# Kernel tuning notes

Measured on AMD Instinct MI355X. Metric: run time of the kernel, lower is better.

Reference implementation:

```python
import jax, jax.numpy as jnp
import numpy as np


def setup_inputs() -> dict:
    key = jax.random.key(0)
    k1, k2 = jax.random.split(key)
    B, C, M, N = 4, 3, 4096, 8192
    query = jax.random.normal(k1, (B, C, M), dtype=jnp.float32)
    points = jax.random.normal(k2, (B, C, N), dtype=jnp.float32)
    return {"k": 16, "query": query, "points": points}


def reference(k, query, points):
    # query: BxCxM, points: BxCxN  (trans=True path of original module)
    q = jnp.swapaxes(query, 1, 2)   # BxMxC
    p = jnp.swapaxes(points, 1, 2)  # BxNxC
    # squared L2 distances (FAISS GpuIndexFlatL2): BxMxN
    q2 = jnp.sum(q * q, axis=-1, keepdims=True)           # BxMx1
    p2 = jnp.sum(p * p, axis=-1)[:, None, :]              # Bx1xN
    dist = q2 + p2 - 2.0 * jnp.einsum('bmc,bnc->bmn', q, p)
    # k smallest distances, sorted ascending (FAISS sorts results)
    _, index_batch = jax.lax.top_k(-dist, k)              # BxMxK int32
    index_batch = index_batch.astype(jnp.int64) if index_batch.dtype != jnp.int64 else index_batch
    # gather neighbor coordinates: points BxCxN, idx BxMxK -> BxCxMxK
    neighbor_points = jax.vmap(lambda pts, idx: pts[:, idx])(points, index_batch)
    return neighbor_points, index_batch
```

## Files before the change

### kernel.cpp

```cpp
#include <hip/hip_runtime.h>
#include <stdint.h>

#define BQ 4
#define CC 3
#define MM 4096
#define NN 8192
#define KK 16
#define NP_OFF (BQ*CC*MM*KK)
#define BLOCK 512
#define ROWS 32
#define CHUNK 1024
#define NCH (NN/CHUNK)
#define EPSA 4e-3f

typedef __attribute__((ext_vector_type(8)))  short   short8;
typedef __attribute__((ext_vector_type(8)))  __bf16  bf16x8;
typedef __attribute__((ext_vector_type(16))) float   f32x16;
typedef unsigned int u32;
typedef unsigned short u16;

#define BT_PER_BATCH 256
#define AT_PER_BATCH 128
#define A_OFF (BQ*BT_PER_BATCH*64)

__device__ __forceinline__ float rfl(float x) {
    return __uint_as_float((unsigned)__builtin_amdgcn_readfirstlane((int)__float_as_uint(x)));
}
__device__ __forceinline__ unsigned mapf(float f) {
    unsigned u = __float_as_uint(f);
    return (u & 0x80000000u) ? ~u : (u | 0x80000000u);
}
__device__ __forceinline__ float unmapf(unsigned u) {
    unsigned b = (u & 0x80000000u) ? (u & 0x7fffffffu) : ~u;
    return __uint_as_float(b);
}
__device__ __forceinline__ u16 bfh(float f) {
    unsigned u = __float_as_uint(f);
    return (u16)((u + 0x7fffu + ((u >> 16) & 1u)) >> 16);
}
__device__ __forceinline__ float bff(u16 h) {
    return __uint_as_float(((unsigned)h) << 16);
}

__device__ __forceinline__ f32x16 mfma3216(short8 a, short8 b, f32x16 c) {
    return __builtin_amdgcn_mfma_f32_32x32x16_bf16(
        __builtin_bit_cast(bf16x8, a), __builtin_bit_cast(bf16x8, b), c, 0, 0, 0);
}

__device__ __forceinline__ void gl_lds16(const void* g, void* l) {
    __builtin_amdgcn_global_load_lds(
        (const __attribute__((address_space(1))) u32*)g,
        (__attribute__((address_space(3))) u32*)l, 16, 0, 0);
}

__global__ void pack_kernel(const float* __restrict__ query,
                            const float* __restrict__ points,
                            short8* __restrict__ ws)
{
    const int lane = threadIdx.x;
    const int bid  = blockIdx.x;
    const int hi   = lane >> 5;
    const int j    = lane & 31;
    short8 v = {0,0,0,0,0,0,0,0};
    if (bid < BQ*BT_PER_BATCH) {
        const int b = bid >> 8, tile = bid & 255;
        const int n = tile*32 + j;
        const float* pb = points + b*(CC*NN);
        float px = pb[n], py = pb[NN+n], pz = pb[2*NN+n];
        float pw = -0.5f*(px*px + py*py + pz*pz);
        u16 xh=bfh(px), yh=bfh(py), zh=bfh(pz), wh=bfh(pw);
        u16 xl=bfh(px-bff(xh)), yl=bfh(py-bff(yh)), zl=bfh(pz-bff(zh)), wl=bfh(pw-bff(wh));
        if (hi == 0) { v[0]=(short)xh; v[1]=(short)xh; v[2]=(short)xl; v[3]=(short)yh;
                       v[4]=(short)zl; v[5]=(short)wh; v[6]=(short)wl; v[7]=0; }
        else         { v[0]=(short)yh; v[1]=(short)yl; v[2]=(short)zh; v[3]=(short)zh; }
        ws[bid*64 + lane] = v;
    } else {
        const int t2 = bid - BQ*BT_PER_BATCH;
        const int b = t2 >> 7, rt = t2 & 127;
        const int m = rt*32 + j;
        const float* qb = query + b*(CC*MM);
        float qx = qb[m], qy = qb[MM+m], qz = qb[2*MM+m];
        u16 xh=bfh(qx), yh=bfh(qy), zh=bfh(qz);
        u16 xl=bfh(qx-bff(xh)), yl=bfh(qy-bff(yh)), zl=bfh(qz-bff(zh));
        const u16 ONE = 0x3F80u;
        if (hi == 0) { v[0]=(short)xh; v[1]=(short)xl; v[2]=(short)xh; v[3]=(short)yh;
                       v[4]=(short)zh; v[5]=(short)ONE; v[6]=(short)ONE; v[7]=0; }
        else         { v[0]=(short)yl; v[1]=(short)yh; v[2]=(short)zh; v[3]=(short)zl; }
        ws[A_OFF + t2*64 + lane] = v;
    }
}

__global__ __launch_bounds__(BLOCK, 4) void knn_kernel(
    const float* __restrict__ query,
    const float* __restrict__ points,
    const short8* __restrict__ ws,
    float* __restrict__ out)
{
    __shared__ short8 bpk[2][2048];
    __shared__ unsigned aux[ROWS][64];
    __shared__ unsigned scnt[ROWS];
    __shared__ unsigned rcbits[ROWS];

    const int tid  = threadIdx.x;
    const int lane = tid & 63;
    const int wv   = tid >> 6;
    const int col  = lane & 31;
    const int hi4  = (lane >> 5) << 2;
    const int bid  = blockIdx.x;
    const int b    = bid >> 7;
    const int rt   = bid & 127;
    const int rb   = rt * 32;

    const float* pb = points + b*(CC*NN);
    const float* qb = query  + b*(CC*MM);

    #pragma unroll
    for (int i = 0; i < 4; ++i) ((unsigned*)aux)[i*BLOCK + tid] = 0u;
    if (tid < ROWS) scnt[tid] = 0u;

    const short8 af = ws[A_OFF + (b*AT_PER_BATCH + rt)*64 + lane];
    const f32x16 zf = {0.f,0.f,0.f,0.f,0.f,0.f,0.f,0.f,
                       0.f,0.f,0.f,0.f,0.f,0.f,0.f,0.f};

    float rm0[16], rm1[16];
    #pragma unroll
    for (int j = 0; j < 16; ++j) { rm0[j] = -__builtin_inff(); rm1[j] = -__builtin_inff(); }

    const short8* Bb = ws + (size_t)b * (BT_PER_BATCH*64);

    auto stage = [&](int ch, int bi) {
        #pragma unroll
        for (int i = 0; i < 4; ++i) {
            int idx = i*BLOCK + tid;
            gl_lds16(&Bb[ch*2048 + idx], &bpk[bi][idx]);
        }
    };

    auto comp1 = [&](int bi) {
        #pragma unroll
        for (int p = 0; p < 2; ++p) {
            short8 b0 = bpk[bi][(wv*4 + p)*64 + lane];
            short8 b1 = bpk[bi][(wv*4 + p + 2)*64 + lane];
            f32x16 d0 = mfma3216(af, b0, zf);
            f32x16 d1 = mfma3216(af, b1, zf);
            #pragma unroll
            for (int j = 0; j < 16; ++j) {
                float t = fmaxf(d0[j], d1[j]);
                if (p == 0) rm0[j] = fmaxf(rm0[j], t);
                else        rm1[j] = fmaxf(rm1[j], t);
            }
        }
    };

    stage(0, 0);
    #pragma unroll 1
    for (int ch = 0; ch < NCH; ch += 2) {
        __syncthreads();
        if (ch + 1 < NCH) stage(ch + 1, 1);
        comp1(0);
        __syncthreads();
        if (ch + 2 < NCH) stage(ch + 2, 0);
        if (ch + 1 < NCH) comp1(1);
    }

    #pragma unroll
    for (int j = 0; j < 16; ++j) {
        int row = ((j & 3) + 8*(j >> 2)) + hi4;
        atomicMax(&aux[row][col],      mapf(rm0[j]));
        atomicMax(&aux[row][col + 32], mapf(rm1[j]));
    }
    __syncthreads();
    stage(0, 0);

    #pragma unroll
    for (int rr = 0; rr < 4; ++rr) {
        int row = wv*4 + rr;
        unsigned v = aux[row][lane];
        #pragma unroll
        for (int k = 2; k <= 64; k <<= 1) {
            #pragma unroll
            for (int jj = k >> 1; jj > 0; jj >>= 1) {
                unsigned o = __shfl_xor(v, jj, 64);
                bool keepmin = (((lane & jj) == 0) == ((lane & k) == 0));
                v = keepmin ? (v < o ? v : o) : (v > o ? v : o);
            }
        }
        unsigned tb = __shfl(v, 48, 64);
        if (lane == 0) rcbits[row] = __float_as_uint(unmapf(tb) - EPSA);
    }
    __syncthreads();

    float rcv[16];
    #pragma unroll
    for (int j = 0; j < 16; ++j)
        rcv[j] = __uint_as_float(rcbits[((j & 3) + 8*(j >> 2)) + hi4]);

    auto comp2 = [&](int ch, int bi) {
        #pragma unroll
        for (int p = 0; p < 2; ++p) {
            short8 b0 = bpk[bi][(wv*4 + p)*64 + lane];
            short8 b1 = bpk[bi][(wv*4 + p + 2)*64 + lane];
            f32x16 d0 = mfma3216(af, b0, zf);
            f32x16 d1 = mfma3216(af, b1, zf);
            unsigned n0 = (unsigned)(ch*CHUNK + (wv*4 + p)*32 + col);
            #pragma unroll
            for (int j = 0; j < 16; ++j) {
                float t = fmaxf(d0[j], d1[j]);
                if (t >= rcv[j]) {
                    int row = ((j & 3) + 8*(j >> 2)) + hi4;
                    if (d0[j] >= rcv[j]) {
                        unsigned pos = atomicAdd(&scnt[row], 1u);
                        if (pos < 64u) aux[row][pos] = n0;
                    }
                    if (d1[j] >= rcv[j]) {
                        unsigned pos = atomicAdd(&scnt[row], 1u);
                        if (pos < 64u) aux[row][pos] = n0 + 64u;
                    }
                }
            }
        }
    };

    #pragma unroll 1
    for (int ch = 0; ch < NCH; ch += 2) {
        __syncthreads();
        if (ch + 1 < NCH) stage(ch + 1, 1);
        comp2(ch, 0);
        __syncthreads();
        if (ch + 2 < NCH) stage(ch + 2, 0);
        if (ch + 1 < NCH) comp2(ch + 1, 1);
    }
    __syncthreads();

    #pragma unroll 1
    for (int rr = 0; rr < 4; ++rr) {
        int row = wv*4 + rr;
        int m   = rb + row;
        float ex = rfl(qb[m]);
        float ey = rfl(qb[MM + m]);
        float ez = rfl(qb[2*MM + m]);
        float eq2 = rfl(__fadd_rn(__fadd_rn(__fmul_rn(ex,ex), __fmul_rn(ey,ey)),
                                  __fmul_rn(ez,ez)));
        unsigned c = scnt[row]; if (c > 64u) c = 64u;
        unsigned kb = 0xffffffffu, id = 0xffffffffu;
        if (lane < (int)c) {
            id = aux[row][lane];
            float px = pb[id], py = pb[NN + id], pz = pb[2*NN + id];
            float p2 = __fadd_rn(__fadd_rn(__fmul_rn(px,px), __fmul_rn(py,py)),
                                 __fmul_rn(pz,pz));
            float dot = __builtin_fmaf(ez, pz,
                         __builtin_fmaf(ey, py, __fmul_rn(ex, px)));
            float d = __fsub_rn(__fadd_rn(eq2, p2), __fmul_rn(2.0f, dot));
            unsigned fb = __float_as_uint(d);
            kb = (fb & 0x80000000u) ? ~fb : (fb | 0x80000000u);
        }
        #pragma unroll
        for (int k = 2; k <= 64; k <<= 1) {
            #pragma unroll
            for (int j = k >> 1; j > 0; j >>= 1) {
                unsigned ok = __shfl_xor(kb, j, 64);
                unsigned oi = __shfl_xor(id, j, 64);
                bool takeMin  = (((lane & j) == 0) == ((lane & k) == 0));
                bool selfLess = (kb < ok) || (kb == ok && id < oi);
                if (selfLess != takeMin) { kb = ok; id = oi; }
            }
        }
        if (lane < KK) {
            int oi = (int)id;
            out[NP_OFF + (b * MM + m) * KK + lane] = (float)oi;
            out[((b * CC + 0) * MM + m) * KK + lane] = pb[oi];
            out[((b * CC + 1) * MM + m) * KK + lane] = pb[NN + oi];
            out[((b * CC + 2) * MM + m) * KK + lane] = pb[2*NN + oi];
        }
    }
}

extern "C" void kernel_launch(void* const* d_in, const int* in_sizes, int n_in,
                              void* d_out, int out_size, void* d_ws, size_t ws_size,
                              hipStream_t stream) {
    const float* query  = (const float*)d_in[1];
    const float* points = (const float*)d_in[2];
    float* out = (float*)d_out;
    short8* ws = (short8*)d_ws;

    pack_kernel<<<dim3(BQ*BT_PER_BATCH + BQ*AT_PER_BATCH), dim3(64), 0, stream>>>(
        query, points, ws);
    knn_kernel<<<dim3(BQ * (MM / ROWS)), dim3(BLOCK), 0, stream>>>(
        query, points, ws, out);
}
```

Measured before the change: 105.0 us.

## Load packed point tiles directly from global per wave, drop LDS staging

Removes the double-buffered LDS staging and its block-wide barriers in both scan passes. Each wave now reads its own contiguous slice of 32 packed point tiles straight from global memory (L2), four tiles per iteration. Query packing moves into the main kernel, the pack kernel uses larger blocks, and block IDs are swizzled so neighbouring blocks spread across batches. This trades shared-memory reuse and barrier cost for more global/L2 traffic and exposed load latency, while freeing LDS for occupancy.

```diff
diff --git a/kernel.cpp b/kernel.cpp
--- a/kernel.cpp
+++ b/kernel.cpp
@@ -9,8 +9,6 @@
 #define NP_OFF (BQ*CC*MM*KK)
 #define BLOCK 512
 #define ROWS 32
-#define CHUNK 1024
-#define NCH (NN/CHUNK)
 #define EPSA 4e-3f
 
 typedef __attribute__((ext_vector_type(8)))  short   short8;
@@ -20,8 +18,7 @@
 typedef unsigned short u16;
 
 #define BT_PER_BATCH 256
-#define AT_PER_BATCH 128
-#define A_OFF (BQ*BT_PER_BATCH*64)
+#define WTILES 32
 
 __device__ __forceinline__ float rfl(float x) {
     return __uint_as_float((unsigned)__builtin_amdgcn_readfirstlane((int)__float_as_uint(x)));
@@ -47,47 +44,26 @@
         __builtin_bit_cast(bf16x8, a), __builtin_bit_cast(bf16x8, b), c, 0, 0, 0);
 }
 
-__device__ __forceinline__ void gl_lds16(const void* g, void* l) {
-    __builtin_amdgcn_global_load_lds(
-        (const __attribute__((address_space(1))) u32*)g,
-        (__attribute__((address_space(3))) u32*)l, 16, 0, 0);
-}
-
-__global__ void pack_kernel(const float* __restrict__ query,
-                            const float* __restrict__ points,
+__global__ void pack_kernel(const float* __restrict__ points,
                             short8* __restrict__ ws)
 {
-    const int lane = threadIdx.x;
-    const int bid  = blockIdx.x;
-    const int hi   = lane >> 5;
-    const int j    = lane & 31;
+    const int g = blockIdx.x * 256 + threadIdx.x;
+    const int lane = g & 63;
+    const int tileIdx = g >> 6;
+    const int b = tileIdx >> 8, tile = tileIdx & 255;
+    const int hi = lane >> 5;
+    const int j = lane & 31;
+    const int n = tile*32 + j;
+    const float* pb = points + b*(CC*NN);
+    float px = pb[n], py = pb[NN+n], pz = pb[2*NN+n];
+    float pw = -0.5f*(px*px + py*py + pz*pz);
+    u16 xh=bfh(px), yh=bfh(py), zh=bfh(pz), wh=bfh(pw);
+    u16 xl=bfh(px-bff(xh)), yl=bfh(py-bff(yh)), zl=bfh(pz-bff(zh)), wl=bfh(pw-bff(wh));
     short8 v = {0,0,0,0,0,0,0,0};
-    if (bid < BQ*BT_PER_BATCH) {
-        const int b = bid >> 8, tile = bid & 255;
-        const int n = tile*32 + j;
-        const float* pb = points + b*(CC*NN);
-        float px = pb[n], py = pb[NN+n], pz = pb[2*NN+n];
-        float pw = -0.5f*(px*px + py*py + pz*pz);
-        u16 xh=bfh(px), yh=bfh(py), zh=bfh(pz), wh=bfh(pw);
-        u16 xl=bfh(px-bff(xh)), yl=bfh(py-bff(yh)), zl=bfh(pz-bff(zh)), wl=bfh(pw-bff(wh));
-        if (hi == 0) { v[0]=(short)xh; v[1]=(short)xh; v[2]=(short)xl; v[3]=(short)yh;
-                       v[4]=(short)zl; v[5]=(short)wh; v[6]=(short)wl; v[7]=0; }
-        else         { v[0]=(short)yh; v[1]=(short)yl; v[2]=(short)zh; v[3]=(short)zh; }
-        ws[bid*64 + lane] = v;
-    } else {
-        const int t2 = bid - BQ*BT_PER_BATCH;
-        const int b = t2 >> 7, rt = t2 & 127;
-        const int m = rt*32 + j;
-        const float* qb = query + b*(CC*MM);
-        float qx = qb[m], qy = qb[MM+m], qz = qb[2*MM+m];
-        u16 xh=bfh(qx), yh=bfh(qy), zh=bfh(qz);
-        u16 xl=bfh(qx-bff(xh)), yl=bfh(qy-bff(yh)), zl=bfh(qz-bff(zh));
-        const u16 ONE = 0x3F80u;
-        if (hi == 0) { v[0]=(short)xh; v[1]=(short)xl; v[2]=(short)xh; v[3]=(short)yh;
-                       v[4]=(short)zh; v[5]=(short)ONE; v[6]=(short)ONE; v[7]=0; }
-        else         { v[0]=(short)yl; v[1]=(short)yh; v[2]=(short)zh; v[3]=(short)zl; }
-        ws[A_OFF + t2*64 + lane] = v;
-    }
+    if (hi == 0) { v[0]=(short)xh; v[1]=(short)xh; v[2]=(short)xl; v[3]=(short)yh;
+                   v[4]=(short)zl; v[5]=(short)wh; v[6]=(short)wl; v[7]=0; }
+    else         { v[0]=(short)yh; v[1]=(short)yl; v[2]=(short)zh; v[3]=(short)zh; }
+    ws[tileIdx*64 + lane] = v;
 }
 
 __global__ __launch_bounds__(BLOCK, 4) void knn_kernel(
@@ -96,7 +72,6 @@
     const short8* __restrict__ ws,
     float* __restrict__ out)
 {
-    __shared__ short8 bpk[2][2048];
     __shared__ unsigned aux[ROWS][64];
     __shared__ unsigned scnt[ROWS];
     __shared__ unsigned rcbits[ROWS];
@@ -107,8 +82,9 @@
     const int col  = lane & 31;
     const int hi4  = (lane >> 5) << 2;
     const int bid  = blockIdx.x;
-    const int b    = bid >> 7;
-    const int rt   = bid & 127;
+    const int lid  = ((bid & 7) << 6) | (bid >> 3);
+    const int b    = lid >> 7;
+    const int rt   = lid & 127;
     const int rb   = rt * 32;
 
     const float* pb = points + b*(CC*NN);
@@ -118,49 +94,47 @@
     for (int i = 0; i < 4; ++i) ((unsigned*)aux)[i*BLOCK + tid] = 0u;
     if (tid < ROWS) scnt[tid] = 0u;
 
-    const short8 af = ws[A_OFF + (b*AT_PER_BATCH + rt)*64 + lane];
+    {
+    }
+    const int jq = lane & 31, hiq = lane >> 5;
+    const int mA = rb + jq;
+    float qxv = qb[mA], qyv = qb[MM+mA], qzv = qb[2*MM+mA];
+    u16 axh=bfh(qxv), ayh=bfh(qyv), azh=bfh(qzv);
+    u16 axl=bfh(qxv-bff(axh)), ayl=bfh(qyv-bff(ayh)), azl=bfh(qzv-bff(azh));
+    const u16 ONE = 0x3F80u;
+    short8 af = {0,0,0,0,0,0,0,0};
+    if (hiq == 0) { af[0]=(short)axh; af[1]=(short)axl; af[2]=(short)axh; af[3]=(short)ayh;
+                    af[4]=(short)azh; af[5]=(short)ONE; af[6]=(short)ONE; }
+    else          { af[0]=(short)ayl; af[1]=(short)ayh; af[2]=(short)azh; af[3]=(short)azl; }
+
     const f32x16 zf = {0.f,0.f,0.f,0.f,0.f,0.f,0.f,0.f,
                        0.f,0.f,0.f,0.f,0.f,0.f,0.f,0.f};
 
+    __syncthreads();
+
     float rm0[16], rm1[16];
     #pragma unroll
     for (int j = 0; j < 16; ++j) { rm0[j] = -__builtin_inff(); rm1[j] = -__builtin_inff(); }
 
-    const short8* Bb = ws + (size_t)b * (BT_PER_BATCH*64);
-
-    auto stage = [&](int ch, int bi) {
-        #pragma unroll
-        for (int i = 0; i < 4; ++i) {
-            int idx = i*BLOCK + tid;
-            gl_lds16(&Bb[ch*2048 + idx], &bpk[bi][idx]);
-        }
-    };
-
-    auto comp1 = [&](int bi) {
-        #pragma unroll
-        for (int p = 0; p < 2; ++p) {
-            short8 b0 = bpk[bi][(wv*4 + p)*64 + lane];
-            short8 b1 = bpk[bi][(wv*4 + p + 2)*64 + lane];
+    {
+        const short8* Wp = ws + ((size_t)b*BT_PER_BATCH + wv*WTILES)*64 + lane;
+        #pragma unroll 1
+        for (int it = 0; it < 8; ++it) {
+            short8 b0 = Wp[0*64];
+            short8 b1 = Wp[1*64];
+            short8 b2 = Wp[2*64];
+            short8 b3 = Wp[3*64];
             f32x16 d0 = mfma3216(af, b0, zf);
+            f32x16 d2 = mfma3216(af, b2, zf);
             f32x16 d1 = mfma3216(af, b1, zf);
+            f32x16 d3 = mfma3216(af, b3, zf);
             #pragma unroll
             for (int j = 0; j < 16; ++j) {
-                float t = fmaxf(d0[j], d1[j]);
-                if (p == 0) rm0[j] = fmaxf(rm0[j], t);
-                else        rm1[j] = fmaxf(rm1[j], t);
-            }
-        }
-    };
-
-    stage(0, 0);
-    #pragma unroll 1
-    for (int ch = 0; ch < NCH; ch += 2) {
-        __syncthreads();
-        if (ch + 1 < NCH) stage(ch + 1, 1);
-        comp1(0);
-        __syncthreads();
-        if (ch + 2 < NCH) stage(ch + 2, 0);
-        if (ch + 1 < NCH) comp1(1);
+                rm0[j] = fmaxf(rm0[j], fmaxf(d0[j], d2[j]));
+                rm1[j] = fmaxf(rm1[j], fmaxf(d1[j], d3[j]));
+            }
+            Wp += 4*64;
+        }
     }
 
     #pragma unroll
@@ -170,7 +144,6 @@
         atomicMax(&aux[row][col + 32], mapf(rm1[j]));
     }
     __syncthreads();
-    stage(0, 0);
 
     #pragma unroll
     for (int rr = 0; rr < 4; ++rr) {
@@ -195,40 +168,45 @@
     for (int j = 0; j < 16; ++j)
         rcv[j] = __uint_as_float(rcbits[((j & 3) + 8*(j >> 2)) + hi4]);
 
-    auto comp2 = [&](int ch, int bi) {
-        #pragma unroll
-        for (int p = 0; p < 2; ++p) {
-            short8 b0 = bpk[bi][(wv*4 + p)*64 + lane];
-            short8 b1 = bpk[bi][(wv*4 + p + 2)*64 + lane];
+    {
+        const short8* Wp = ws + ((size_t)b*BT_PER_BATCH + wv*WTILES)*64 + lane;
+        unsigned nbase = (unsigned)(wv*WTILES*32 + col);
+        #pragma unroll 1
+        for (int it = 0; it < 8; ++it) {
+            short8 b0 = Wp[0*64];
+            short8 b1 = Wp[1*64];
+            short8 b2 = Wp[2*64];
+            short8 b3 = Wp[3*64];
             f32x16 d0 = mfma3216(af, b0, zf);
             f32x16 d1 = mfma3216(af, b1, zf);
-            unsigned n0 = (unsigned)(ch*CHUNK + (wv*4 + p)*32 + col);
+            f32x16 d2 = mfma3216(af, b2, zf);
+            f32x16 d3 = mfma3216(af, b3, zf);
             #pragma unroll
             for (int j = 0; j < 16; ++j) {
-                float t = fmaxf(d0[j], d1[j]);
-                if (t >= rcv[j]) {
+                float tm = fmaxf(fmaxf(d0[j], d1[j]), fmaxf(d2[j], d3[j]));
+                if (tm >= rcv[j]) {
                     int row = ((j & 3) + 8*(j >> 2)) + hi4;
                     if (d0[j] >= rcv[j]) {
                         unsigned pos = atomicAdd(&scnt[row], 1u);
-                        if (pos < 64u) aux[row][pos] = n0;
+                        if (pos < 64u) aux[row][pos] = nbase;
                     }
                     if (d1[j] >= rcv[j]) {
                         unsigned pos = atomicAdd(&scnt[row], 1u);
-                        if (pos < 64u) aux[row][pos] = n0 + 64u;
+                        if (pos < 64u) aux[row][pos] = nbase + 32u;
+                    }
+                    if (d2[j] >= rcv[j]) {
+                        unsigned pos = atomicAdd(&scnt[row], 1u);
+                        if (pos < 64u) aux[row][pos] = nbase + 64u;
+                    }
+                    if (d3[j] >= rcv[j]) {
+                        unsigned pos = atomicAdd(&scnt[row], 1u);
+                        if (pos < 64u) aux[row][pos] = nbase + 96u;
                     }
                 }
             }
-        }
-    };
-
-    #pragma unroll 1
-    for (int ch = 0; ch < NCH; ch += 2) {
-        __syncthreads();
-        if (ch + 1 < NCH) stage(ch + 1, 1);
-        comp2(ch, 0);
-        __syncthreads();
-        if (ch + 2 < NCH) stage(ch + 2, 0);
-        if (ch + 1 < NCH) comp2(ch + 1, 1);
+            Wp += 4*64;
+            nbase += 128u;
+        }
     }
     __syncthreads();
 
@@ -283,8 +261,7 @@
     float* out = (float*)d_out;
     short8* ws = (short8*)d_ws;
 
-    pack_kernel<<<dim3(BQ*BT_PER_BATCH + BQ*AT_PER_BATCH), dim3(64), 0, stream>>>(
-        query, points, ws);
+    pack_kernel<<<dim3(256), dim3(256), 0, stream>>>(points, ws);
     knn_kernel<<<dim3(BQ * (MM / ROWS)), dim3(BLOCK), 0, stream>>>(
         query, points, ws, out);
 }
```

After: 98.48 us. 6.2% less time.
